# Optimization experiments

Measured on AMD Instinct MI355X. Metric: run time of the kernel, lower is better.

## Reference

```python
import jax, jax.numpy as jnp
import numpy as np

B, P, E = 16, 1024, 768
HID, HEADS = 768, 12
DH = HID // HEADS  # 64
EPS = 1e-5


def setup_inputs() -> dict:
    key = jax.random.key(0)
    ks = jax.random.split(key, 4)
    return {
        "x": jax.random.normal(ks[0], (B, P, E), dtype=jnp.float32),
        "ln_weight": jnp.ones((P, E), dtype=jnp.float32),
        "ln_bias": jnp.zeros((P, E), dtype=jnp.float32),
        "qkv": jax.random.normal(ks[1], (E, 3 * HID), dtype=jnp.float32),
        "lin_w": jax.random.normal(ks[2], (HID, E), dtype=jnp.float32) * 0.02,
        "lin_b": jax.random.normal(ks[3], (E,), dtype=jnp.float32) * 0.02,
    }


def reference(x, ln_weight, ln_bias, qkv, lin_w, lin_b):
    # LayerNorm over the last TWO dims (patches, emb), per torch nn.LayerNorm((P, E))
    mean = jnp.mean(x, axis=(-2, -1), keepdims=True)
    var = jnp.var(x, axis=(-2, -1), keepdims=True)
    xn = (x - mean) / jnp.sqrt(var + EPS) * ln_weight + ln_bias

    # QKV projection: [B,P,E] @ [E,3*HID] -> [B,P,3*HID]
    proj = xn @ qkv
    # view(B,P,heads,-1) then permute -> [B,heads,P,3*DH]; chunk along last dim
    proj = proj.reshape(B, P, HEADS, 3 * DH).transpose(0, 2, 1, 3)
    q, k, v = proj[..., :DH], proj[..., DH:2 * DH], proj[..., 2 * DH:]

    # Softmax-free attention: (Q K^T) V
    atten = jnp.einsum("bhqd,bhkd->bhqk", q, k)  # [B,H,P,P]
    out = jnp.einsum("bhqk,bhkd->bhqd", atten, v)  # [B,H,P,DH]

    out = out.transpose(0, 2, 1, 3).reshape(B, P, HID)
    # dropout p=0.0 (eval) -> identity
    out = jax.nn.relu(out @ lin_w + lin_b)
    return out + x
```

## Files before the change

kernel.cpp:

```cpp
#include <hip/hip_runtime.h>
#include <hip/hip_bf16.h>
#include <cstdint>

#define BB   16
#define PP   1024
#define EE   768
#define HID  768
#define NH   12
#define DH   64
#define NPB  (PP * EE)
#define MROWS (BB * PP)

typedef __bf16 bf16_t;
typedef __bf16 bf16x8 __attribute__((ext_vector_type(8)));
typedef float  f32x4  __attribute__((ext_vector_type(4)));

__device__ __forceinline__ void gld16(const void* g, void* l) {
    __builtin_amdgcn_global_load_lds(
        (const __attribute__((address_space(1))) void*)(uintptr_t)g,
        (__attribute__((address_space(3))) void*)(uint32_t)(uintptr_t)l,
        16, 0, 0);
}

__global__ __launch_bounds__(256) void stats1_kernel(const float* __restrict__ x,
                                                     float* __restrict__ part) {
    int bid = blockIdx.x;
    int b = bid >> 6, s = bid & 63;
    const float4* xp = (const float4*)(x + (size_t)b * NPB + (size_t)s * 12288);
    float sum = 0.f, ss = 0.f;
#pragma unroll
    for (int i = 0; i < 12; ++i) {
        float4 v = xp[i * 256 + threadIdx.x];
        sum += v.x + v.y + v.z + v.w;
        ss  += v.x * v.x + v.y * v.y + v.z * v.z + v.w * v.w;
    }
#pragma unroll
    for (int off = 32; off > 0; off >>= 1) {
        sum += __shfl_down(sum, off, 64);
        ss  += __shfl_down(ss,  off, 64);
    }
    __shared__ float tmp[8];
    int wave = threadIdx.x >> 6, lane = threadIdx.x & 63;
    if (lane == 0) { tmp[wave * 2] = sum; tmp[wave * 2 + 1] = ss; }
    __syncthreads();
    if (threadIdx.x == 0) {
        part[bid * 2]     = tmp[0] + tmp[2] + tmp[4] + tmp[6];
        part[bid * 2 + 1] = tmp[1] + tmp[3] + tmp[5] + tmp[7];
    }
}

__global__ __launch_bounds__(256) void prep_kernel(const float* __restrict__ qkvw,
                                                   const float* __restrict__ linw,
                                                   const float* __restrict__ part,
                                                   bf16_t* __restrict__ qkvT,
                                                   bf16_t* __restrict__ lwT,
                                                   float* __restrict__ stats) {
    int bid = blockIdx.x;
    if (bid < 576) {
        __shared__ float lds[64][65];
        const float* src; bf16_t* dst; int r0, c0, W;
        if (bid < 432) {
            int tr = bid / 36, tc = bid - tr * 36;
            r0 = tr * 64; c0 = tc * 64; src = qkvw; W = 2304; dst = qkvT;
        } else {
            int bb = bid - 432;
            int tr = bb / 12, tc = bb - tr * 12;
            r0 = tr * 64; c0 = tc * 64; src = linw; W = 768; dst = lwT;
        }
        int t = threadIdx.x;
        int rr = t >> 4, cc4 = (t & 15) * 4;
#pragma unroll
        for (int j = 0; j < 4; ++j) {
            float4 v = *(const float4*)(src + (size_t)(r0 + rr + j * 16) * W + c0 + cc4);
            lds[rr + j * 16][cc4 + 0] = v.x;
            lds[rr + j * 16][cc4 + 1] = v.y;
            lds[rr + j * 16][cc4 + 2] = v.z;
            lds[rr + j * 16][cc4 + 3] = v.w;
        }
        __syncthreads();
        int cl = t >> 3, rgl = (t & 7) * 8;
#pragma unroll
        for (int jj = 0; jj < 2; ++jj) {
            int c = jj * 32 + cl;
            union { bf16_t h[8]; uint4 u; } o;
#pragma unroll
            for (int k = 0; k < 8; ++k) o.h[k] = (bf16_t)lds[rgl + k][c];
            *(uint4*)(dst + (size_t)(c0 + c) * 768 + r0 + rgl) = o.u;
        }
    } else {
        int wave = threadIdx.x >> 6, lane = threadIdx.x & 63;
#pragma unroll
        for (int j = 0; j < 4; ++j) {
            int b = wave * 4 + j;
            float sum = part[(b * 64 + lane) * 2];
            float ss  = part[(b * 64 + lane) * 2 + 1];
#pragma unroll
            for (int off = 32; off > 0; off >>= 1) {
                sum += __shfl_down(sum, off, 64);
                ss  += __shfl_down(ss,  off, 64);
            }
            if (lane == 0) {
                const float inv_n = 1.f / (float)NPB;
                float mean = sum * inv_n;
                float var  = ss * inv_n - mean * mean;
                stats[b * 2]     = mean;
                stats[b * 2 + 1] = rsqrtf(var + 1e-5f);
            }
        }
    }
}

__global__ __launch_bounds__(256) void ln_apply_kernel(const float* __restrict__ x,
                                                       const float* __restrict__ lnw,
                                                       const float* __restrict__ lnb,
                                                       const float* __restrict__ stats,
                                                       bf16_t* __restrict__ xn) {
    int i = (blockIdx.x * 256 + threadIdx.x) * 8;
    int b = i / NPB;
    int r = i - b * NPB;
    float mean = stats[b * 2], rstd = stats[b * 2 + 1];
    float4 x0 = *(const float4*)(x + i),     x1 = *(const float4*)(x + i + 4);
    float4 w0 = *(const float4*)(lnw + r),   w1 = *(const float4*)(lnw + r + 4);
    float4 c0 = *(const float4*)(lnb + r),   c1 = *(const float4*)(lnb + r + 4);
    union { bf16_t h[8]; uint4 u; } o;
    o.h[0] = (bf16_t)((x0.x - mean) * rstd * w0.x + c0.x);
    o.h[1] = (bf16_t)((x0.y - mean) * rstd * w0.y + c0.y);
    o.h[2] = (bf16_t)((x0.z - mean) * rstd * w0.z + c0.z);
    o.h[3] = (bf16_t)((x0.w - mean) * rstd * w0.w + c0.w);
    o.h[4] = (bf16_t)((x1.x - mean) * rstd * w1.x + c1.x);
    o.h[5] = (bf16_t)((x1.y - mean) * rstd * w1.y + c1.y);
    o.h[6] = (bf16_t)((x1.z - mean) * rstd * w1.z + c1.z);
    o.h[7] = (bf16_t)((x1.w - mean) * rstd * w1.w + c1.w);
    *(uint4*)(xn + i) = o.u;
}

__device__ __forceinline__ void core128_bk32(const bf16_t* __restrict__ A,
                                             const bf16_t* __restrict__ Bt,
                                             int mBase, int nBase,
                                             f32x4 acc[4][4], bf16_t* smem) {
    const int t = threadIdx.x, lane = t & 63, wave = t >> 6;
    const int wm = wave >> 1, wn = wave & 1;
    const int m16 = lane & 15, quad = lane >> 4;

    const bf16_t* gsrc[4];
    int ldst[4];
#pragma unroll
    for (int j = 0; j < 2; ++j) {
        int c = t + 256 * j;
        int l = c >> 3, lg = ((c & 7) - (l & 7)) & 7;
        int row = l + (lg >> 2) * 64, kc = lg & 3;
        gsrc[j]     = A  + (size_t)(mBase + row) * 768 + kc * 8;
        ldst[j]     = c * 8;
        gsrc[2 + j] = Bt + (size_t)(nBase + row) * 768 + kc * 8;
        ldst[2 + j] = 4096 + c * 8;
    }

    int aOff[4], bOff[4];
#pragma unroll
    for (int f = 0; f < 4; ++f) {
        aOff[f] = (f * 16 + m16) * 64 + (((wm * 4 + quad) + (m16 & 7)) & 7) * 8;
        bOff[f] = 4096 + (f * 16 + m16) * 64 + (((wn * 4 + quad) + (m16 & 7)) & 7) * 8;
    }

    const f32x4 z = {0.f, 0.f, 0.f, 0.f};
#pragma unroll
    for (int mf = 0; mf < 4; ++mf)
#pragma unroll
        for (int nf = 0; nf < 4; ++nf) acc[mf][nf] = z;

#pragma unroll
    for (int j = 0; j < 4; ++j) gld16(gsrc[j], smem + ldst[j]);
#pragma unroll
    for (int j = 0; j < 4; ++j) gld16(gsrc[j] + 32, smem + 8192 + ldst[j]);

#pragma unroll
    for (int step = 0; step < 24; ++step) {
        const int cur = (step % 3) * 8192;
        asm volatile("s_waitcnt lgkmcnt(0)" ::: "memory");
        __builtin_amdgcn_sched_barrier(0);
        __builtin_amdgcn_s_barrier();
        if (step + 2 < 24) {
            const int nb = ((step + 2) % 3) * 8192;
            const int kq = (step + 2) * 32;
#pragma unroll
            for (int j = 0; j < 4; ++j)
                gld16(gsrc[j] + kq, smem + nb + ldst[j]);
        }
        if (step < 22)       asm volatile("s_waitcnt vmcnt(8)" ::: "memory");
        else if (step == 22) asm volatile("s_waitcnt vmcnt(4)" ::: "memory");
        else                 asm volatile("s_waitcnt vmcnt(0)" ::: "memory");
        __builtin_amdgcn_sched_barrier(0);
        __builtin_amdgcn_s_barrier();

        bf16x8 af[4], bfv[4];
#pragma unroll
        for (int f = 0; f < 4; ++f) {
            af[f]  = *(const bf16x8*)(smem + cur + aOff[f]);
            bfv[f] = *(const bf16x8*)(smem + cur + bOff[f]);
        }
        __builtin_amdgcn_s_setprio(1);
#pragma unroll
        for (int mf = 0; mf < 4; ++mf)
#pragma unroll
            for (int nf = 0; nf < 4; ++nf)
                acc[mf][nf] = __builtin_amdgcn_mfma_f32_16x16x32_bf16(
                    af[mf], bfv[nf], acc[mf][nf], 0, 0, 0);
        __builtin_amdgcn_s_setprio(0);
    }
}

__global__ __launch_bounds__(256, 3) void gemm_qkv_kernel(const bf16_t* __restrict__ xn,
                                                          const bf16_t* __restrict__ qkvT,
                                                          bf16_t* __restrict__ q,
                                                          bf16_t* __restrict__ kt,
                                                          bf16_t* __restrict__ vt) {
    __shared__ bf16_t smem[24576];
    const int t = threadIdx.x, lane = t & 63, wave = t >> 6;
    const int wm = wave >> 1, wn = wave & 1;
    const int m16 = lane & 15, quad = lane >> 4;

    const int lb = blockIdx.y * 18 + blockIdx.x;
    const int id = (lb & 7) * 288 + (lb >> 3);
    const int tx = id % 18, ty = id / 18;
    const int mBase = ty * 128, nBase = tx * 128;

    f32x4 acc[4][4];
    core128_bk32(xn, qkvT, mBase, nBase, acc, smem);

    __syncthreads();
    bf16_t* slot = smem + wave * 4608;
    const int b = mBase >> 10, p0 = mBase & 1023;
    const int g64 = tx * 2 + wn;
    const int cls = g64 % 3, h = g64 / 3;

    if (cls == 0) {
#pragma unroll
        for (int mf = 0; mf < 4; ++mf)
#pragma unroll
            for (int nf = 0; nf < 4; ++nf)
#pragma unroll
                for (int i = 0; i < 4; ++i)
                    slot[(mf * 16 + quad * 4 + i) * 72 + nf * 16 + m16] =
                        (bf16_t)acc[mf][nf][i];
        asm volatile("s_waitcnt lgkmcnt(0)" ::: "memory");
        __builtin_amdgcn_sched_barrier(0);
#pragma unroll
        for (int j = 0; j < 8; ++j) {
            int r = j * 8 + (lane >> 3), cc = lane & 7;
            bf16x8 val = *(const bf16x8*)(slot + r * 72 + cc * 8);
            *(bf16x8*)(q + ((size_t)(b * 1024 + p0 + wm * 64 + r)) * 768 +
                       h * 64 + cc * 8) = val;
        }
    } else {
        bf16_t* dst = (cls == 1) ? kt : vt;
        const size_t bh = (size_t)(b * 12 + h);
#pragma unroll
        for (int mf = 0; mf < 4; ++mf)
#pragma unroll
            for (int nf = 0; nf < 4; ++nf) {
                int c = nf * 16 + m16;
                union { bf16_t hh[4]; uint2 u; } pk;
#pragma unroll
                for (int i = 0; i < 4; ++i) pk.hh[i] = (bf16_t)acc[mf][nf][i];
                *(uint2*)(slot + c * 72 + mf * 16 + quad * 4) = pk.u;
            }
        asm volatile("s_waitcnt lgkmcnt(0)" ::: "memory");
        __builtin_amdgcn_sched_barrier(0);
#pragma unroll
        for (int j = 0; j < 8; ++j) {
            int c = (lane >> 3) + j * 8, r8 = (lane & 7) * 8;
            bf16x8 val = *(const bf16x8*)(slot + c * 72 + r8);
            *(bf16x8*)(dst + (bh * 64 + c) * 1024 + p0 + wm * 64 + r8) = val;
        }
    }
}

__global__ __launch_bounds__(256) void kvu_kernel(const bf16_t* __restrict__ kt,
                                                  const bf16_t* __restrict__ vt,
                                                  const bf16_t* __restrict__ lwT,
                                                  bf16_t* __restrict__ ut) {
    __shared__ float red[4 * 64 * 65];
    const int bh = blockIdx.x;
    const int b = bh / NH, h = bh - b * NH;
    const bf16_t* Kb = kt + (size_t)bh * DH * PP;
    const bf16_t* Vb = vt + (size_t)bh * DH * PP;
    const int t = threadIdx.x;
    const int lane = t & 63, wave = t >> 6;
    const int m16 = lane & 15, quad = lane >> 4;
    const f32x4 z = {0.f, 0.f, 0.f, 0.f};

    {
        f32x4 acc[4][4];
#pragma unroll
        for (int mm = 0; mm < 4; ++mm)
#pragma unroll
            for (int nn = 0; nn < 4; ++nn) acc[mm][nn] = z;
        for (int ks = 0; ks < 8; ++ks) {
            int kb = wave * 256 + ks * 32 + quad * 8;
            bf16x8 af[4], bfv[4];
#pragma unroll
            for (int mm = 0; mm < 4; ++mm)
                af[mm] = *(const bf16x8*)(Kb + (size_t)(mm * 16 + m16) * PP + kb);
#pragma unroll
            for (int nn = 0; nn < 4; ++nn)
                bfv[nn] = *(const bf16x8*)(Vb + (size_t)(nn * 16 + m16) * PP + kb);
#pragma unroll
            for (int mm = 0; mm < 4; ++mm)
#pragma unroll
                for (int nn = 0; nn < 4; ++nn)
                    acc[mm][nn] = __builtin_amdgcn_mfma_f32_16x16x32_bf16(
                        af[mm], bfv[nn], acc[mm][nn], 0, 0, 0);
        }
#pragma unroll
        for (int mm = 0; mm < 4; ++mm)
#pragma unroll
            for (int nn = 0; nn < 4; ++nn)
#pragma unroll
                for (int i = 0; i < 4; ++i)
                    red[wave * 4160 + (mm * 16 + quad * 4 + i) * 65 + nn * 16 + m16] =
                        acc[mm][nn][i];
    }
    __syncthreads();

    const int wm = wave >> 1, wn = wave & 1;
    bf16x8 ah[2][2], al[2][2];
#pragma unroll
    for (int mm = 0; mm < 2; ++mm)
#pragma unroll
        for (int ks = 0; ks < 2; ++ks) {
            int d1 = wm * 32 + mm * 16 + m16;
            int base = d1 * 65 + ks * 32 + quad * 8;
#pragma unroll
            for (int e = 0; e < 8; ++e) {
                float s = red[base + e] + red[4160 + base + e] +
                          red[8320 + base + e] + red[12480 + base + e];
                bf16_t hi = (bf16_t)s;
                ah[mm][ks][e] = hi;
                al[mm][ks][e] = (bf16_t)(s - (float)hi);
            }
        }

#pragma unroll
    for (int ny = 0; ny < 3; ++ny) {
        const int nBase = ny * 256;
        f32x4 acc2[2][8];
#pragma unroll
        for (int mm = 0; mm < 2; ++mm)
#pragma unroll
            for (int nn = 0; nn < 8; ++nn) acc2[mm][nn] = z;
#pragma unroll
        for (int ks = 0; ks < 2; ++ks) {
            bf16x8 bfr[8];
#pragma unroll
            for (int nn = 0; nn < 8; ++nn)
                bfr[nn] = *(const bf16x8*)(
                    lwT + (size_t)(nBase + wn * 128 + nn * 16 + m16) * 768 +
                    h * 64 + ks * 32 + quad * 8);
#pragma unroll
            for (int mm = 0; mm < 2; ++mm)
#pragma unroll
                for (int nn = 0; nn < 8; ++nn) {
                    acc2[mm][nn] = __builtin_amdgcn_mfma_f32_16x16x32_bf16(
                        ah[mm][ks], bfr[nn], acc2[mm][nn], 0, 0, 0);
                    acc2[mm][nn] = __builtin_amdgcn_mfma_f32_16x16x32_bf16(
                        al[mm][ks], bfr[nn], acc2[mm][nn], 0, 0, 0);
                }
        }
#pragma unroll
        for (int mm = 0; mm < 2; ++mm)
#pragma unroll
            for (int nn = 0; nn < 8; ++nn) {
                int e  = nBase + wn * 128 + nn * 16 + m16;
                int d1 = wm * 32 + mm * 16 + quad * 4;
                union { bf16_t hh[4]; uint2 u; } pk;
#pragma unroll
                for (int i = 0; i < 4; ++i) pk.hh[i] = (bf16_t)acc2[mm][nn][i];
                *(uint2*)(ut + ((size_t)b * 768 + e) * 768 + h * 64 + d1) = pk.u;
            }
    }
}

__global__ __launch_bounds__(256, 3) void gemm_out_kernel(const bf16_t* __restrict__ q,
                                                          const bf16_t* __restrict__ ut,
                                                          const float* __restrict__ linb,
                                                          const float* __restrict__ x,
                                                          float* __restrict__ out) {
    __shared__ bf16_t smem[24576];
    const int lb  = blockIdx.y * 6 + blockIdx.x;
    const int swz = (lb & 7) * 96 + (lb >> 3);
    const int tx  = swz % 6, ty = swz / 6;
    const int mBase = ty * 128, nBase = tx * 128;
    const int b = mBase >> 10;

    f32x4 acc[4][4];
    core128_bk32(q, ut + (size_t)b * 768 * 768, mBase, nBase, acc, smem);

    const int lane = threadIdx.x & 63, wave = threadIdx.x >> 6;
    const int wm = wave >> 1, wn = wave & 1;
    const int m16 = lane & 15, quad = lane >> 4;
#pragma unroll
    for (int mm = 0; mm < 4; ++mm) {
#pragma unroll
        for (int i = 0; i < 4; ++i) {
            size_t row = mBase + wm * 64 + mm * 16 + quad * 4 + i;
#pragma unroll
            for (int nn = 0; nn < 4; ++nn) {
                int col = nBase + wn * 64 + nn * 16 + m16;
                float v = acc[mm][nn][i] + linb[col];
                v = fmaxf(v, 0.f) + x[row * EE + col];
                out[row * EE + col] = v;
            }
        }
    }
}

extern "C" void kernel_launch(void* const* d_in, const int* in_sizes, int n_in,
                              void* d_out, int out_size, void* d_ws, size_t ws_size,
                              hipStream_t stream) {
    const float* x    = (const float*)d_in[0];
    const float* lnw  = (const float*)d_in[1];
    const float* lnb  = (const float*)d_in[2];
    const float* qkvw = (const float*)d_in[3];
    const float* linw = (const float*)d_in[4];
    const float* linb = (const float*)d_in[5];
    float* out = (float*)d_out;
    char* ws = (char*)d_ws;

    float*  part  = (float*)(ws + 0);
    float*  stats = (float*)(ws + 8192);
    bf16_t* xn    = (bf16_t*)(ws + 8448);
    bf16_t* qkvT  = (bf16_t*)(ws + 25174272);
    bf16_t* lwT   = (bf16_t*)(ws + 28713216);
    bf16_t* q     = (bf16_t*)(ws + 29892864);
    bf16_t* kt    = (bf16_t*)(ws + 55058688);
    bf16_t* vt    = (bf16_t*)(ws + 80224512);
    bf16_t* ut    = xn;

    stats1_kernel<<<dim3(BB * 64), dim3(256), 0, stream>>>(x, part);
    prep_kernel<<<dim3(577), dim3(256), 0, stream>>>(qkvw, linw, part, qkvT, lwT, stats);
    ln_apply_kernel<<<dim3(6144), dim3(256), 0, stream>>>(x, lnw, lnb, stats, xn);
    gemm_qkv_kernel<<<dim3(18, 128), dim3(256), 0, stream>>>(xn, qkvT, q, kt, vt);
    kvu_kernel<<<dim3(192), dim3(256), 0, stream>>>(kt, vt, lwT, ut);
    gemm_out_kernel<<<dim3(6, 128), dim3(256), 0, stream>>>(q, ut, linb, x, out);
}
```

Measured before the change: 251.9 us.

## Enlarge GEMM tiles to 256x256 with 8-wave blocks for QKV and output GEMMs

Result: slower. 257.7 us (+2.3%).

```diff
diff --git a/kernel.cpp b/kernel.cpp
--- a/kernel.cpp
+++ b/kernel.cpp
@@ -134,53 +134,58 @@
     *(uint4*)(xn + i) = o.u;
 }
 
-__device__ __forceinline__ void core128_bk32(const bf16_t* __restrict__ A,
+__device__ __forceinline__ void core256_bk32(const bf16_t* __restrict__ A,
                                              const bf16_t* __restrict__ Bt,
                                              int mBase, int nBase,
-                                             f32x4 acc[4][4], bf16_t* smem) {
+                                             f32x4 acc[8][4], bf16_t* smem) {
     const int t = threadIdx.x, lane = t & 63, wave = t >> 6;
-    const int wm = wave >> 1, wn = wave & 1;
+    const int wm = wave >> 2, wn = wave & 3;
     const int m16 = lane & 15, quad = lane >> 4;
 
     const bf16_t* gsrc[4];
     int ldst[4];
 #pragma unroll
     for (int j = 0; j < 2; ++j) {
-        int c = t + 256 * j;
+        int c = t + 512 * j;
         int l = c >> 3, lg = ((c & 7) - (l & 7)) & 7;
-        int row = l + (lg >> 2) * 64, kc = lg & 3;
+        int row = l + (lg >> 2) * 128, kc = lg & 3;
         gsrc[j]     = A  + (size_t)(mBase + row) * 768 + kc * 8;
         ldst[j]     = c * 8;
         gsrc[2 + j] = Bt + (size_t)(nBase + row) * 768 + kc * 8;
-        ldst[2 + j] = 4096 + c * 8;
-    }
-
-    int aOff[4], bOff[4];
-#pragma unroll
-    for (int f = 0; f < 4; ++f) {
-        aOff[f] = (f * 16 + m16) * 64 + (((wm * 4 + quad) + (m16 & 7)) & 7) * 8;
-        bOff[f] = 4096 + (f * 16 + m16) * 64 + (((wn * 4 + quad) + (m16 & 7)) & 7) * 8;
+        ldst[2 + j] = 8192 + c * 8;
+    }
+
+    int aOff[8], bOff[4];
+#pragma unroll
+    for (int mf = 0; mf < 8; ++mf) {
+        int l = mf * 16 + m16;
+        aOff[mf] = l * 64 + (((wm * 4 + quad) + (l & 7)) & 7) * 8;
+    }
+#pragma unroll
+    for (int nf = 0; nf < 4; ++nf) {
+        int l = (wn & 1) * 64 + nf * 16 + m16;
+        bOff[nf] = 8192 + l * 64 + ((((wn >> 1) * 4 + quad) + (l & 7)) & 7) * 8;
     }
 
     const f32x4 z = {0.f, 0.f, 0.f, 0.f};
 #pragma unroll
-    for (int mf = 0; mf < 4; ++mf)
+    for (int mf = 0; mf < 8; ++mf)
 #pragma unroll
         for (int nf = 0; nf < 4; ++nf) acc[mf][nf] = z;
 
 #pragma unroll
     for (int j = 0; j < 4; ++j) gld16(gsrc[j], smem + ldst[j]);
 #pragma unroll
-    for (int j = 0; j < 4; ++j) gld16(gsrc[j] + 32, smem + 8192 + ldst[j]);
+    for (int j = 0; j < 4; ++j) gld16(gsrc[j] + 32, smem + 16384 + ldst[j]);
 
 #pragma unroll
     for (int step = 0; step < 24; ++step) {
-        const int cur = (step % 3) * 8192;
+        const int cur = (step % 3) * 16384;
         asm volatile("s_waitcnt lgkmcnt(0)" ::: "memory");
         __builtin_amdgcn_sched_barrier(0);
         __builtin_amdgcn_s_barrier();
         if (step + 2 < 24) {
-            const int nb = ((step + 2) % 3) * 8192;
+            const int nb = ((step + 2) % 3) * 16384;
             const int kq = (step + 2) * 32;
 #pragma unroll
             for (int j = 0; j < 4; ++j)
@@ -192,85 +197,101 @@
         __builtin_amdgcn_sched_barrier(0);
         __builtin_amdgcn_s_barrier();
 
-        bf16x8 af[4], bfv[4];
-#pragma unroll
-        for (int f = 0; f < 4; ++f) {
-            af[f]  = *(const bf16x8*)(smem + cur + aOff[f]);
-            bfv[f] = *(const bf16x8*)(smem + cur + bOff[f]);
-        }
+        bf16x8 af0[4], bfv[4], af1[4];
+#pragma unroll
+        for (int f = 0; f < 4; ++f) af0[f] = *(const bf16x8*)(smem + cur + aOff[f]);
+#pragma unroll
+        for (int f = 0; f < 4; ++f) bfv[f] = *(const bf16x8*)(smem + cur + bOff[f]);
+#pragma unroll
+        for (int f = 0; f < 4; ++f) af1[f] = *(const bf16x8*)(smem + cur + aOff[4 + f]);
         __builtin_amdgcn_s_setprio(1);
 #pragma unroll
         for (int mf = 0; mf < 4; ++mf)
 #pragma unroll
             for (int nf = 0; nf < 4; ++nf)
                 acc[mf][nf] = __builtin_amdgcn_mfma_f32_16x16x32_bf16(
-                    af[mf], bfv[nf], acc[mf][nf], 0, 0, 0);
+                    af0[mf], bfv[nf], acc[mf][nf], 0, 0, 0);
+#pragma unroll
+        for (int mf = 0; mf < 4; ++mf)
+#pragma unroll
+            for (int nf = 0; nf < 4; ++nf)
+                acc[4 + mf][nf] = __builtin_amdgcn_mfma_f32_16x16x32_bf16(
+                    af1[mf], bfv[nf], acc[4 + mf][nf], 0, 0, 0);
         __builtin_amdgcn_s_setprio(0);
     }
 }
 
-__global__ __launch_bounds__(256, 3) void gemm_qkv_kernel(const bf16_t* __restrict__ xn,
+__global__ __launch_bounds__(512, 2) void gemm_qkv_kernel(const bf16_t* __restrict__ xn,
                                                           const bf16_t* __restrict__ qkvT,
                                                           bf16_t* __restrict__ q,
                                                           bf16_t* __restrict__ kt,
                                                           bf16_t* __restrict__ vt) {
-    __shared__ bf16_t smem[24576];
+    __shared__ bf16_t smem[49152];
     const int t = threadIdx.x, lane = t & 63, wave = t >> 6;
-    const int wm = wave >> 1, wn = wave & 1;
+    const int wm = wave >> 2, wn = wave & 3;
     const int m16 = lane & 15, quad = lane >> 4;
 
-    const int lb = blockIdx.y * 18 + blockIdx.x;
-    const int id = (lb & 7) * 288 + (lb >> 3);
-    const int tx = id % 18, ty = id / 18;
-    const int mBase = ty * 128, nBase = tx * 128;
-
-    f32x4 acc[4][4];
-    core128_bk32(xn, qkvT, mBase, nBase, acc, smem);
+    const int lb = blockIdx.y * 9 + blockIdx.x;
+    const int id = (lb & 7) * 72 + (lb >> 3);
+    const int tx = id % 9, ty = id / 9;
+    const int mBase = ty * 256, nBase = tx * 256;
+
+    f32x4 acc[8][4];
+    core256_bk32(xn, qkvT, mBase, nBase, acc, smem);
 
     __syncthreads();
     bf16_t* slot = smem + wave * 4608;
     const int b = mBase >> 10, p0 = mBase & 1023;
-    const int g64 = tx * 2 + wn;
+    const int g64 = tx * 4 + wn;
     const int cls = g64 % 3, h = g64 / 3;
 
-    if (cls == 0) {
-#pragma unroll
-        for (int mf = 0; mf < 4; ++mf)
-#pragma unroll
-            for (int nf = 0; nf < 4; ++nf)
-#pragma unroll
-                for (int i = 0; i < 4; ++i)
-                    slot[(mf * 16 + quad * 4 + i) * 72 + nf * 16 + m16] =
-                        (bf16_t)acc[mf][nf][i];
-        asm volatile("s_waitcnt lgkmcnt(0)" ::: "memory");
-        __builtin_amdgcn_sched_barrier(0);
-#pragma unroll
-        for (int j = 0; j < 8; ++j) {
-            int r = j * 8 + (lane >> 3), cc = lane & 7;
-            bf16x8 val = *(const bf16x8*)(slot + r * 72 + cc * 8);
-            *(bf16x8*)(q + ((size_t)(b * 1024 + p0 + wm * 64 + r)) * 768 +
-                       h * 64 + cc * 8) = val;
-        }
-    } else {
-        bf16_t* dst = (cls == 1) ? kt : vt;
-        const size_t bh = (size_t)(b * 12 + h);
-#pragma unroll
-        for (int mf = 0; mf < 4; ++mf)
-#pragma unroll
-            for (int nf = 0; nf < 4; ++nf) {
-                int c = nf * 16 + m16;
-                union { bf16_t hh[4]; uint2 u; } pk;
-#pragma unroll
-                for (int i = 0; i < 4; ++i) pk.hh[i] = (bf16_t)acc[mf][nf][i];
-                *(uint2*)(slot + c * 72 + mf * 16 + quad * 4) = pk.u;
-            }
-        asm volatile("s_waitcnt lgkmcnt(0)" ::: "memory");
-        __builtin_amdgcn_sched_barrier(0);
-#pragma unroll
-        for (int j = 0; j < 8; ++j) {
-            int c = (lane >> 3) + j * 8, r8 = (lane & 7) * 8;
-            bf16x8 val = *(const bf16x8*)(slot + c * 72 + r8);
-            *(bf16x8*)(dst + (bh * 64 + c) * 1024 + p0 + wm * 64 + r8) = val;
+#pragma unroll
+    for (int pass = 0; pass < 2; ++pass) {
+        if (cls == 0) {
+#pragma unroll
+            for (int mf = 0; mf < 4; ++mf)
+#pragma unroll
+                for (int nf = 0; nf < 4; ++nf)
+#pragma unroll
+                    for (int i = 0; i < 4; ++i)
+                        slot[(mf * 16 + quad * 4 + i) * 72 + nf * 16 + m16] =
+                            (bf16_t)acc[pass * 4 + mf][nf][i];
+            asm volatile("s_waitcnt lgkmcnt(0)" ::: "memory");
+            __builtin_amdgcn_sched_barrier(0);
+#pragma unroll
+            for (int j = 0; j < 8; ++j) {
+                int r = j * 8 + (lane >> 3), cc = lane & 7;
+                bf16x8 val = *(const bf16x8*)(slot + r * 72 + cc * 8);
+                *(bf16x8*)(q + ((size_t)(b * 1024 + p0 + wm * 128 + pass * 64 + r)) * 768 +
+                           h * 64 + cc * 8) = val;
+            }
+        } else {
+            bf16_t* dst = (cls == 1) ? kt : vt;
+            const size_t bh = (size_t)(b * 12 + h);
+#pragma unroll
+            for (int mf = 0; mf < 4; ++mf)
+#pragma unroll
+                for (int nf = 0; nf < 4; ++nf) {
+                    int c = nf * 16 + m16;
+                    union { bf16_t hh[4]; uint2 u; } pk;
+#pragma unroll
+                    for (int i = 0; i < 4; ++i)
+                        pk.hh[i] = (bf16_t)acc[pass * 4 + mf][nf][i];
+                    *(uint2*)(slot + c * 72 + mf * 16 + quad * 4) = pk.u;
+                }
+            asm volatile("s_waitcnt lgkmcnt(0)" ::: "memory");
+            __builtin_amdgcn_sched_barrier(0);
+#pragma unroll
+            for (int j = 0; j < 8; ++j) {
+                int c = (lane >> 3) + j * 8, r8 = (lane & 7) * 8;
+                bf16x8 val = *(const bf16x8*)(slot + c * 72 + r8);
+                *(bf16x8*)(dst + (bh * 64 + c) * 1024 + p0 + wm * 128 +
+                           pass * 64 + r8) = val;
+            }
+        }
+        if (pass == 0) {
+            asm volatile("s_waitcnt lgkmcnt(0)" ::: "memory");
+            __builtin_amdgcn_sched_barrier(0);
         }
     }
 }
@@ -380,33 +401,33 @@
     }
 }
 
-__global__ __launch_bounds__(256, 3) void gemm_out_kernel(const bf16_t* __restrict__ q,
+__global__ __launch_bounds__(512, 2) void gemm_out_kernel(const bf16_t* __restrict__ q,
                                                           const bf16_t* __restrict__ ut,
                                                           const float* __restrict__ linb,
                                                           const float* __restrict__ x,
                                                           float* __restrict__ out) {
-    __shared__ bf16_t smem[24576];
-    const int lb  = blockIdx.y * 6 + blockIdx.x;
-    const int swz = (lb & 7) * 96 + (lb >> 3);
-    const int tx  = swz % 6, ty = swz / 6;
-    const int mBase = ty * 128, nBase = tx * 128;
+    __shared__ bf16_t smem[49152];
+    const int lb = blockIdx.y * 3 + blockIdx.x;
+    const int id = (lb & 7) * 24 + (lb >> 3);
+    const int tx = id % 3, ty = id / 3;
+    const int mBase = ty * 256, nBase = tx * 256;
     const int b = mBase >> 10;
 
-    f32x4 acc[4][4];
-    core128_bk32(q, ut + (size_t)b * 768 * 768, mBase, nBase, acc, smem);
+    f32x4 acc[8][4];
+    core256_bk32(q, ut + (size_t)b * 768 * 768, mBase, nBase, acc, smem);
 
     const int lane = threadIdx.x & 63, wave = threadIdx.x >> 6;
-    const int wm = wave >> 1, wn = wave & 1;
+    const int wm = wave >> 2, wn = wave & 3;
     const int m16 = lane & 15, quad = lane >> 4;
 #pragma unroll
-    for (int mm = 0; mm < 4; ++mm) {
+    for (int mf = 0; mf < 8; ++mf) {
 #pragma unroll
         for (int i = 0; i < 4; ++i) {
-            size_t row = mBase + wm * 64 + mm * 16 + quad * 4 + i;
-#pragma unroll
-            for (int nn = 0; nn < 4; ++nn) {
-                int col = nBase + wn * 64 + nn * 16 + m16;
-                float v = acc[mm][nn][i] + linb[col];
+            size_t row = mBase + wm * 128 + mf * 16 + quad * 4 + i;
+#pragma unroll
+            for (int nf = 0; nf < 4; ++nf) {
+                int col = nBase + wn * 64 + nf * 16 + m16;
+                float v = acc[mf][nf][i] + linb[col];
                 v = fmaxf(v, 0.f) + x[row * EE + col];
                 out[row * EE + col] = v;
             }
@@ -439,7 +460,7 @@
     stats1_kernel<<<dim3(BB * 64), dim3(256), 0, stream>>>(x, part);
     prep_kernel<<<dim3(577), dim3(256), 0, stream>>>(qkvw, linw, part, qkvT, lwT, stats);
     ln_apply_kernel<<<dim3(6144), dim3(256), 0, stream>>>(x, lnw, lnb, stats, xn);
-    gemm_qkv_kernel<<<dim3(18, 128), dim3(256), 0, stream>>>(xn, qkvT, q, kt, vt);
+    gemm_qkv_kernel<<<dim3(9, 64), dim3(512), 0, stream>>>(xn, qkvT, q, kt, vt);
     kvu_kernel<<<dim3(192), dim3(256), 0, stream>>>(kt, vt, lwT, ut);
-    gemm_out_kernel<<<dim3(6, 128), dim3(256), 0, stream>>>(q, ut, linb, x, out);
-}
+    gemm_out_kernel<<<dim3(3, 64), dim3(512), 0, stream>>>(q, ut, linb, x, out);
+}
```

## Widen QKV GEMM tile to 128x256 and stage output epilogue through LDS

Applied to the files above, without the earlier changes.

Result: faster. 244.7 us (-2.9%).

```diff
diff --git a/kernel.cpp b/kernel.cpp
--- a/kernel.cpp
+++ b/kernel.cpp
@@ -209,68 +209,159 @@
     }
 }
 
-__global__ __launch_bounds__(256, 3) void gemm_qkv_kernel(const bf16_t* __restrict__ xn,
+__global__ __launch_bounds__(256, 2) void gemm_qkv_kernel(const bf16_t* __restrict__ xn,
                                                           const bf16_t* __restrict__ qkvT,
                                                           bf16_t* __restrict__ q,
                                                           bf16_t* __restrict__ kt,
                                                           bf16_t* __restrict__ vt) {
-    __shared__ bf16_t smem[24576];
+    __shared__ bf16_t smem[36864];
     const int t = threadIdx.x, lane = t & 63, wave = t >> 6;
     const int wm = wave >> 1, wn = wave & 1;
     const int m16 = lane & 15, quad = lane >> 4;
 
-    const int lb = blockIdx.y * 18 + blockIdx.x;
-    const int id = (lb & 7) * 288 + (lb >> 3);
-    const int tx = id % 18, ty = id / 18;
-    const int mBase = ty * 128, nBase = tx * 128;
-
-    f32x4 acc[4][4];
-    core128_bk32(xn, qkvT, mBase, nBase, acc, smem);
-
-    __syncthreads();
+    const int lb = blockIdx.y * 9 + blockIdx.x;
+    const int id = (lb & 7) * 144 + (lb >> 3);
+    const int tx = id % 9, ty = id / 9;
+    const int mBase = ty * 128, nBase = tx * 256;
+
+    const bf16_t* gsrc[6];
+    int ldst[6];
+#pragma unroll
+    for (int j = 0; j < 2; ++j) {
+        int c = t + 256 * j;
+        int l = c >> 3, lg = ((c & 7) - (l & 7)) & 7;
+        gsrc[j] = xn + (size_t)(mBase + l + (lg >> 2) * 64) * 768 + (lg & 3) * 8;
+        ldst[j] = c * 8;
+    }
+#pragma unroll
+    for (int j = 0; j < 4; ++j) {
+        int c = t + 256 * j;
+        int l = c >> 3, lg = ((c & 7) - (l & 7)) & 7;
+        gsrc[2 + j] = qkvT + (size_t)(nBase + l + (lg >> 2) * 128) * 768 + (lg & 3) * 8;
+        ldst[2 + j] = 4096 + c * 8;
+    }
+
+    int aOff[4], bOff[8];
+#pragma unroll
+    for (int mf = 0; mf < 4; ++mf)
+        aOff[mf] = (mf * 16 + m16) * 64 + (((wm * 4 + quad) + (m16 & 7)) & 7) * 8;
+#pragma unroll
+    for (int nf = 0; nf < 8; ++nf)
+        bOff[nf] = 4096 + (nf * 16 + m16) * 64 + (((wn * 4 + quad) + (m16 & 7)) & 7) * 8;
+
+    f32x4 acc[4][8];
+    const f32x4 z = {0.f, 0.f, 0.f, 0.f};
+#pragma unroll
+    for (int mf = 0; mf < 4; ++mf)
+#pragma unroll
+        for (int nf = 0; nf < 8; ++nf) acc[mf][nf] = z;
+
+#pragma unroll
+    for (int j = 0; j < 6; ++j) gld16(gsrc[j], smem + ldst[j]);
+#pragma unroll
+    for (int j = 0; j < 6; ++j) gld16(gsrc[j] + 32, smem + 12288 + ldst[j]);
+
+#pragma unroll
+    for (int step = 0; step < 24; ++step) {
+        const int cur = (step % 3) * 12288;
+        asm volatile("s_waitcnt lgkmcnt(0)" ::: "memory");
+        __builtin_amdgcn_sched_barrier(0);
+        __builtin_amdgcn_s_barrier();
+        if (step + 2 < 24) {
+            const int nb = ((step + 2) % 3) * 12288;
+            const int kq = (step + 2) * 32;
+#pragma unroll
+            for (int j = 0; j < 6; ++j)
+                gld16(gsrc[j] + kq, smem + nb + ldst[j]);
+        }
+        if (step < 22)       asm volatile("s_waitcnt vmcnt(12)" ::: "memory");
+        else if (step == 22) asm volatile("s_waitcnt vmcnt(6)"  ::: "memory");
+        else                 asm volatile("s_waitcnt vmcnt(0)"  ::: "memory");
+        __builtin_amdgcn_sched_barrier(0);
+        __builtin_amdgcn_s_barrier();
+
+        bf16x8 af[4], bf0[4], bf1[4];
+#pragma unroll
+        for (int mf = 0; mf < 4; ++mf)
+            af[mf] = *(const bf16x8*)(smem + cur + aOff[mf]);
+#pragma unroll
+        for (int nf = 0; nf < 4; ++nf)
+            bf0[nf] = *(const bf16x8*)(smem + cur + bOff[nf]);
+        __builtin_amdgcn_s_setprio(1);
+#pragma unroll
+        for (int mf = 0; mf < 4; ++mf)
+#pragma unroll
+            for (int nf = 0; nf < 4; ++nf)
+                acc[mf][nf] = __builtin_amdgcn_mfma_f32_16x16x32_bf16(
+                    af[mf], bf0[nf], acc[mf][nf], 0, 0, 0);
+        __builtin_amdgcn_s_setprio(0);
+        __builtin_amdgcn_s_barrier();
+#pragma unroll
+        for (int nf = 0; nf < 4; ++nf)
+            bf1[nf] = *(const bf16x8*)(smem + cur + bOff[4 + nf]);
+        __builtin_amdgcn_s_setprio(1);
+#pragma unroll
+        for (int mf = 0; mf < 4; ++mf)
+#pragma unroll
+            for (int nf = 0; nf < 4; ++nf)
+                acc[mf][4 + nf] = __builtin_amdgcn_mfma_f32_16x16x32_bf16(
+                    af[mf], bf1[nf], acc[mf][4 + nf], 0, 0, 0);
+        __builtin_amdgcn_s_setprio(0);
+    }
+
+    asm volatile("s_waitcnt lgkmcnt(0)" ::: "memory");
+    __builtin_amdgcn_sched_barrier(0);
     bf16_t* slot = smem + wave * 4608;
     const int b = mBase >> 10, p0 = mBase & 1023;
-    const int g64 = tx * 2 + wn;
-    const int cls = g64 % 3, h = g64 / 3;
-
-    if (cls == 0) {
-#pragma unroll
-        for (int mf = 0; mf < 4; ++mf)
-#pragma unroll
-            for (int nf = 0; nf < 4; ++nf)
-#pragma unroll
-                for (int i = 0; i < 4; ++i)
-                    slot[(mf * 16 + quad * 4 + i) * 72 + nf * 16 + m16] =
-                        (bf16_t)acc[mf][nf][i];
-        asm volatile("s_waitcnt lgkmcnt(0)" ::: "memory");
-        __builtin_amdgcn_sched_barrier(0);
-#pragma unroll
-        for (int j = 0; j < 8; ++j) {
-            int r = j * 8 + (lane >> 3), cc = lane & 7;
-            bf16x8 val = *(const bf16x8*)(slot + r * 72 + cc * 8);
-            *(bf16x8*)(q + ((size_t)(b * 1024 + p0 + wm * 64 + r)) * 768 +
-                       h * 64 + cc * 8) = val;
-        }
-    } else {
-        bf16_t* dst = (cls == 1) ? kt : vt;
-        const size_t bh = (size_t)(b * 12 + h);
-#pragma unroll
-        for (int mf = 0; mf < 4; ++mf)
-#pragma unroll
-            for (int nf = 0; nf < 4; ++nf) {
-                int c = nf * 16 + m16;
-                union { bf16_t hh[4]; uint2 u; } pk;
-#pragma unroll
-                for (int i = 0; i < 4; ++i) pk.hh[i] = (bf16_t)acc[mf][nf][i];
-                *(uint2*)(slot + c * 72 + mf * 16 + quad * 4) = pk.u;
+
+#pragma unroll
+    for (int half = 0; half < 2; ++half) {
+        const int g64 = tx * 4 + wn * 2 + half;
+        const int cls = g64 % 3, h = g64 / 3;
+        if (cls == 0) {
+#pragma unroll
+            for (int mf = 0; mf < 4; ++mf)
+#pragma unroll
+                for (int nfl = 0; nfl < 4; ++nfl)
+#pragma unroll
+                    for (int i = 0; i < 4; ++i)
+                        slot[(mf * 16 + quad * 4 + i) * 72 + nfl * 16 + m16] =
+                            (bf16_t)acc[mf][half * 4 + nfl][i];
+            asm volatile("s_waitcnt lgkmcnt(0)" ::: "memory");
+            __builtin_amdgcn_sched_barrier(0);
+#pragma unroll
+            for (int j = 0; j < 8; ++j) {
+                int r = j * 8 + (lane >> 3), cc = lane & 7;
+                bf16x8 val = *(const bf16x8*)(slot + r * 72 + cc * 8);
+                *(bf16x8*)(q + ((size_t)(b * 1024 + p0 + wm * 64 + r)) * 768 +
+                           h * 64 + cc * 8) = val;
             }
-        asm volatile("s_waitcnt lgkmcnt(0)" ::: "memory");
-        __builtin_amdgcn_sched_barrier(0);
-#pragma unroll
-        for (int j = 0; j < 8; ++j) {
-            int c = (lane >> 3) + j * 8, r8 = (lane & 7) * 8;
-            bf16x8 val = *(const bf16x8*)(slot + c * 72 + r8);
-            *(bf16x8*)(dst + (bh * 64 + c) * 1024 + p0 + wm * 64 + r8) = val;
+        } else {
+            bf16_t* dst = (cls == 1) ? kt : vt;
+            const size_t bh = (size_t)(b * 12 + h);
+#pragma unroll
+            for (int mf = 0; mf < 4; ++mf)
+#pragma unroll
+                for (int nfl = 0; nfl < 4; ++nfl) {
+                    int c = nfl * 16 + m16;
+                    union { bf16_t hh[4]; uint2 u; } pk;
+#pragma unroll
+                    for (int i = 0; i < 4; ++i)
+                        pk.hh[i] = (bf16_t)acc[mf][half * 4 + nfl][i];
+                    *(uint2*)(slot + c * 72 + mf * 16 + quad * 4) = pk.u;
+                }
+            asm volatile("s_waitcnt lgkmcnt(0)" ::: "memory");
+            __builtin_amdgcn_sched_barrier(0);
+#pragma unroll
+            for (int j = 0; j < 8; ++j) {
+                int c = (lane >> 3) + j * 8, r8 = (lane & 7) * 8;
+                bf16x8 val = *(const bf16x8*)(slot + c * 72 + r8);
+                *(bf16x8*)(dst + (bh * 64 + c) * 1024 + p0 + wm * 64 + r8) = val;
+            }
+        }
+        if (half == 0) {
+            asm volatile("s_waitcnt lgkmcnt(0)" ::: "memory");
+            __builtin_amdgcn_sched_barrier(0);
         }
     }
 }
@@ -398,18 +489,44 @@
     const int lane = threadIdx.x & 63, wave = threadIdx.x >> 6;
     const int wm = wave >> 1, wn = wave & 1;
     const int m16 = lane & 15, quad = lane >> 4;
-#pragma unroll
-    for (int mm = 0; mm < 4; ++mm) {
-#pragma unroll
-        for (int i = 0; i < 4; ++i) {
-            size_t row = mBase + wm * 64 + mm * 16 + quad * 4 + i;
-#pragma unroll
-            for (int nn = 0; nn < 4; ++nn) {
-                int col = nBase + wn * 64 + nn * 16 + m16;
-                float v = acc[mm][nn][i] + linb[col];
-                v = fmaxf(v, 0.f) + x[row * EE + col];
-                out[row * EE + col] = v;
-            }
+
+    asm volatile("s_waitcnt lgkmcnt(0)" ::: "memory");
+    __builtin_amdgcn_sched_barrier(0);
+    __syncthreads();
+
+    float* fslot = (float*)smem + wave * 2176;
+    const int cl = lane & 15, rq = lane >> 4;
+    const int colBase = nBase + wn * 64;
+    const float4 lb4 = *(const float4*)(linb + colBase + cl * 4);
+
+#pragma unroll
+    for (int p = 0; p < 2; ++p) {
+#pragma unroll
+        for (int mm = 0; mm < 2; ++mm)
+#pragma unroll
+            for (int nn = 0; nn < 4; ++nn)
+#pragma unroll
+                for (int i = 0; i < 4; ++i)
+                    fslot[(mm * 16 + quad * 4 + i) * 68 + nn * 16 + m16] =
+                        acc[p * 2 + mm][nn][i];
+        asm volatile("s_waitcnt lgkmcnt(0)" ::: "memory");
+        __builtin_amdgcn_sched_barrier(0);
+#pragma unroll
+        for (int j = 0; j < 8; ++j) {
+            int lr = j * 4 + rq;
+            size_t row = (size_t)(mBase + wm * 64 + p * 32 + lr);
+            float4 v4 = *(const float4*)(fslot + lr * 68 + cl * 4);
+            float4 x4 = *(const float4*)(x + row * EE + colBase + cl * 4);
+            float4 o4;
+            o4.x = fmaxf(v4.x + lb4.x, 0.f) + x4.x;
+            o4.y = fmaxf(v4.y + lb4.y, 0.f) + x4.y;
+            o4.z = fmaxf(v4.z + lb4.z, 0.f) + x4.z;
+            o4.w = fmaxf(v4.w + lb4.w, 0.f) + x4.w;
+            *(float4*)(out + row * EE + colBase + cl * 4) = o4;
+        }
+        if (p == 0) {
+            asm volatile("s_waitcnt lgkmcnt(0)" ::: "memory");
+            __builtin_amdgcn_sched_barrier(0);
         }
     }
 }
@@ -439,7 +556,7 @@
     stats1_kernel<<<dim3(BB * 64), dim3(256), 0, stream>>>(x, part);
     prep_kernel<<<dim3(577), dim3(256), 0, stream>>>(qkvw, linw, part, qkvT, lwT, stats);
     ln_apply_kernel<<<dim3(6144), dim3(256), 0, stream>>>(x, lnw, lnb, stats, xn);
-    gemm_qkv_kernel<<<dim3(18, 128), dim3(256), 0, stream>>>(xn, qkvT, q, kt, vt);
+    gemm_qkv_kernel<<<dim3(9, 128), dim3(256), 0, stream>>>(xn, qkvT, q, kt, vt);
     kvu_kernel<<<dim3(192), dim3(256), 0, stream>>>(kt, vt, lwT, ut);
     gemm_out_kernel<<<dim3(6, 128), dim3(256), 0, stream>>>(q, ut, linb, x, out);
 }
```
